# Kernel optimization log

Hardware: AMD Instinct MI355X
Metric: run time of the kernel (lower is better)

## Reference

```python
import jax, jax.numpy as jnp
import numpy as np

EPS = 1e-5       # InstanceNorm1d default eps
TEMP = 1.0       # temperature
SCALE = 8
# (name, arity) of the symbolic base, repeated SCALE times -> 48 functions, layer_size = 64
BASE = [("add", 2), ("mul", 2), ("sin", 1), ("cos", 1), ("tanh", 1), ("identity", 1)]


def _apply(name, a):
    if name == "add":
        return a[0] + a[1]
    if name == "mul":
        return a[0] * a[1]
    if name == "sin":
        return jnp.sin(a[0])
    if name == "cos":
        return jnp.cos(a[0])
    if name == "tanh":
        return jnp.tanh(a[0])
    return a[0]  # identity


def _inorm(x):
    # InstanceNorm1d, affine=False, biased variance, per (sample, channel) over L
    m = jnp.mean(x, axis=-1, keepdims=True)
    v = jnp.var(x, axis=-1, keepdims=True)
    return (x - m) * jax.lax.rsqrt(v + EPS)


def setup_inputs() -> dict:
    key = jax.random.key(0)
    k1, k2, k3 = jax.random.split(key, 3)
    x = jax.random.normal(k1, (64, 256, 4096), dtype=jnp.float32)
    w_channel = 0.1 * jax.random.normal(k2, (64, 256), dtype=jnp.float32)   # channel_conv 1x1
    w_down = 0.1 * jax.random.normal(k3, (48, 256), dtype=jnp.float32)      # down_conv 1x1
    return {"x": x, "w_channel": w_channel, "w_down": w_down}


def reference(x, w_channel, w_down):
    funcs = BASE * SCALE
    nx = _inorm(x)                                   # [B, C, L]
    # forward softmaxes channel_conv weight over output-channel dim (dim=0)
    w_eff = jax.nn.softmax(w_channel / TEMP, axis=0)  # [layer_size, C]
    multi = jnp.einsum("oc,bcl->bol", w_eff, nx)      # [B, layer_size, L]
    args_idx = 0
    output = None
    for i, (name, arity) in enumerate(funcs):
        args = [multi[:, args_idx + j : args_idx + j + 1] for j in range(arity)]
        img = _apply(name, args)                      # [B, 1, L]
        output = img if i == 0 else jnp.concatenate([output, img], axis=1)
        # original re-applies InstanceNorm to the growing tensor each iteration
        output = _inorm(output)
        args_idx += arity
    # skip connection
    output = output + jnp.einsum("oc,bcl->bol", w_down, nx)  # [B, 48, L]
    return output
```

## Files before the change

kernel.cpp:

```cpp
#include <hip/hip_runtime.h>
#include <hip/hip_bf16.h>

#define EPS 1e-5f

typedef unsigned int u32;
typedef unsigned short u16;
typedef __attribute__((ext_vector_type(8))) short bf16x8;
typedef __attribute__((ext_vector_type(4))) float f32x4;

__device__ __forceinline__ u32 f2bf(float f) {
    u32 u = __float_as_uint(f);
    u += 0x7FFFu + ((u >> 16) & 1u);
    return u >> 16;
}
__device__ __forceinline__ float bf2f(u32 h) {
    return __uint_as_float(h << 16);
}

__global__ __launch_bounds__(256) void k1_tstats(const float* __restrict__ x,
                                                 u16* __restrict__ xT,
                                                 float* __restrict__ gS,
                                                 float* __restrict__ gSS) {
    int b  = blockIdx.y;
    int c0 = (blockIdx.x & 7) * 32;
    int l0 = (blockIdx.x >> 3) * 512;
    int t  = threadIdx.x;
    __shared__ __align__(16) u16 T[512 * 32];

    int crow = t >> 3;
    int f4b  = t & 7;
    const float* xr = x + ((size_t)(b * 256 + c0 + crow)) * 4096 + l0;
    int cb   = (2 * crow) & 15;
    int slot = crow >> 3;
    float s = 0.f, ss = 0.f;
#pragma unroll
    for (int i = 0; i < 16; ++i) {
        int f4 = f4b + 8 * i;
        float4 v = *(const float4*)(xr + 4 * f4);
        s  += v.x + v.y + v.z + v.w;
        ss += v.x * v.x + v.y * v.y + v.z * v.z + v.w * v.w;
        char* base = (char*)T + f4 * 256 + (((slot ^ (f4 & 3)) << 4) | cb);
        *(u16*)(base      ) = (u16)f2bf(v.x);
        *(u16*)(base +  64) = (u16)f2bf(v.y);
        *(u16*)(base + 128) = (u16)f2bf(v.z);
        *(u16*)(base + 192) = (u16)f2bf(v.w);
    }
    s += __shfl_xor(s, 1, 64); ss += __shfl_xor(ss, 1, 64);
    s += __shfl_xor(s, 2, 64); ss += __shfl_xor(ss, 2, 64);
    s += __shfl_xor(s, 4, 64); ss += __shfl_xor(ss, 4, 64);
    if ((t & 7) == 0) {
        atomicAdd(&gS [b * 256 + c0 + crow], s);
        atomicAdd(&gSS[b * 256 + c0 + crow], ss);
    }
    __syncthreads();
    u16* xrow = xT + ((size_t)b * 4096 + l0) * 256 + c0;
    int sslot = t & 3;
#pragma unroll
    for (int k = 0; k < 8; ++k) {
        int ll  = k * 64 + (t >> 2);
        int key = (ll >> 2) & 3;
        uint4 vv = *(const uint4*)((const char*)T + ll * 64 + ((sslot ^ key) << 4));
        *(uint4*)(xrow + (size_t)ll * 256 + 8 * sslot) = vv;
    }
}

__global__ __launch_bounds__(256) void k2_prep(const float* __restrict__ wch,
                                               const float* __restrict__ wdn,
                                               const float* __restrict__ gS,
                                               const float* __restrict__ gSS,
                                               u16* __restrict__ Wc,
                                               float* __restrict__ bias,
                                               float* __restrict__ gsum,
                                               float* __restrict__ gss) {
    int b = blockIdx.x, t = threadIdx.x;
    __shared__ float smx[256], sinv[256], ssc[256], smn[256];
    {
        int c = t;
        float mx = -1e30f;
        for (int o = 0; o < 64; ++o) mx = fmaxf(mx, wch[o * 256 + c]);
        float sum = 0.f;
        for (int o = 0; o < 64; ++o) sum += __expf(wch[o * 256 + c] - mx);
        smx[c] = mx; sinv[c] = 1.f / sum;
        float S = gS[b * 256 + c], Q = gSS[b * 256 + c];
        float m = S * (1.f / 4096.f);
        float v = fmaxf(Q * (1.f / 4096.f) - m * m, 0.f);
        ssc[c] = rsqrtf(v + EPS);
        smn[c] = m;
    }
    __syncthreads();

    int lane = t & 63, w = t >> 6;
    int sub = lane >> 5, li = lane & 31;
    int c8 = li * 8;
    u16* Wb = Wc + (size_t)b * 128 * 256;
#pragma unroll 4
    for (int j = 0; j < 16; ++j) {
        int r = j * 8 + w * 2 + sub;
        float p = 0.f;
        u32 packed[4];
#pragma unroll
        for (int e = 0; e < 4; ++e) {
            u32 lohi[2];
#pragma unroll
            for (int h = 0; h < 2; ++h) {
                int c = c8 + 2 * e + h;
                float wv;
                if (r < 64)       wv = __expf(wch[r * 256 + c] - smx[c]) * sinv[c];
                else if (r < 112) wv = wdn[(r - 64) * 256 + c];
                else              wv = 0.f;
                u32 hb = f2bf(wv * ssc[c]);
                lohi[h] = hb;
                p += bf2f(hb) * smn[c];
            }
            packed[e] = lohi[0] | (lohi[1] << 16);
        }
        *(uint4*)&Wb[r * 256 + c8] = *(uint4*)packed;
#pragma unroll
        for (int off = 1; off <= 16; off <<= 1) p += __shfl_xor(p, off, 64);
        if (li == 0) bias[b * 128 + r] = -p;
    }
    if (t < 48) { gsum[b * 48 + t] = 0.f; gss[b * 48 + t] = 0.f; }
}

__global__ __launch_bounds__(256, 4) void k3_main(const u16* __restrict__ xT,
                                                  const u16* __restrict__ Wc,
                                                  const float* __restrict__ bias,
                                                  u16* __restrict__ imgw,
                                                  u16* __restrict__ skipw,
                                                  float* __restrict__ gsum,
                                                  float* __restrict__ gss) {
    int lt = blockIdx.x;
    int b  = blockIdx.y;
    int n0blk = lt * 128;
    int t = threadIdx.x;
    int w = t >> 6, u = t & 63;
    int lane16 = u & 15, q = u >> 4;
    int m0  = (w & 1) * 64;
    int n0w = (w >> 1) * 64;

    __shared__ __align__(16) u16 Wl[128 * 64];
    __shared__ __align__(16) u16 Xl[128 * 64];
    __shared__ float sbias[128];

    if (t < 128) sbias[t] = bias[b * 128 + t];

    f32x4 acc[4][4];
#pragma unroll
    for (int mt = 0; mt < 4; ++mt)
#pragma unroll
        for (int nt = 0; nt < 4; ++nt) acc[mt][nt] = (f32x4){0.f, 0.f, 0.f, 0.f};

    const char* Wb = (const char*)(Wc + (size_t)b * 128 * 256);
    const char* xb = (const char*)(xT + ((size_t)b * 4096 + n0blk) * 256);

    int r0   = t >> 3;
    int jb   = (t & 7) << 4;
    int swz0 = jb ^ (((t >> 3) & 7) << 4);
    int swz16 = (lane16 & 7) << 4;

    for (int cc = 0; cc < 4; ++cc) {
        if (cc) __syncthreads();
        int c0b = cc << 7;
#pragma unroll
        for (int p = 0; p < 4; ++p) {
            int r = r0 + 32 * p;
            uint4 wv = *(const uint4*)(Wb + (size_t)r * 512 + c0b + jb);
            uint4 xv = *(const uint4*)(xb + (size_t)r * 512 + c0b + jb);
            *(uint4*)((char*)Wl + r * 128 + swz0) = wv;
            *(uint4*)((char*)Xl + r * 128 + swz0) = xv;
        }
        __syncthreads();
#pragma unroll
        for (int kk = 0; kk < 2; ++kk) {
            int kob = (kk * 64 + q * 16) ^ swz16;
            bf16x8 af[4], bfr[4];
#pragma unroll
            for (int mt = 0; mt < 4; ++mt)
                af[mt] = *(const bf16x8*)((const char*)Wl + (m0 + 16 * mt + lane16) * 128 + kob);
#pragma unroll
            for (int nt = 0; nt < 4; ++nt)
                bfr[nt] = *(const bf16x8*)((const char*)Xl + (n0w + 16 * nt + lane16) * 128 + kob);
#pragma unroll
            for (int mt = 0; mt < 4; ++mt)
#pragma unroll
                for (int nt = 0; nt < 4; ++nt)
                    acc[mt][nt] = __builtin_amdgcn_mfma_f32_16x16x32_bf16(af[mt], bfr[nt], acc[mt][nt], 0, 0, 0);
        }
    }
    __syncthreads();

    int jb48 = b * 48;
    if (m0 == 0) {
        int g2 = q >> 1, qo = q & 1;
#pragma unroll
        for (int mt = 0; mt < 4; ++mt) {
            int g = 2 * mt + g2;
            int j0 = 6 * g + (qo ? 2 : 0);
            int cnt = qo ? 4 : 2;
            float b0 = sbias[16 * mt + 4 * q + 0];
            float b1 = sbias[16 * mt + 4 * q + 1];
            float b2 = sbias[16 * mt + 4 * q + 2];
            float b3 = sbias[16 * mt + 4 * q + 3];
            float sj[4] = {0.f, 0.f, 0.f, 0.f};
            float qj[4] = {0.f, 0.f, 0.f, 0.f};
#pragma unroll
            for (int nt = 0; nt < 4; ++nt) {
                f32x4 a = acc[mt][nt];
                float a0 = a[0] + b0, a1 = a[1] + b1, a2 = a[2] + b2, a3 = a[3] + b3;
                int n = n0blk + n0w + 16 * nt + lane16;
                float v[4];
                if (!qo) {
                    v[0] = a0 + a1;
                    v[1] = a2 * a3;
                    v[2] = 0.f; v[3] = 0.f;
                } else {
                    v[0] = __sinf(a0);
                    v[1] = __cosf(a1);
                    float e = __expf(-2.f * fabsf(a2));
                    v[2] = copysignf((1.f - e) / (1.f + e), a2);
                    v[3] = a3;
                }
                for (int i = 0; i < cnt; ++i) {
                    imgw[(size_t)(jb48 + j0 + i) * 4096 + n] = (u16)f2bf(v[i]);
                    sj[i] += v[i];
                    qj[i] += v[i] * v[i];
                }
            }
#pragma unroll
            for (int off = 1; off <= 8; off <<= 1) {
#pragma unroll
                for (int i = 0; i < 4; ++i) {
                    sj[i] += __shfl_xor(sj[i], off, 64);
                    qj[i] += __shfl_xor(qj[i], off, 64);
                }
            }
            if (lane16 == 0) {
                for (int i = 0; i < cnt; ++i) {
                    atomicAdd(&gsum[jb48 + j0 + i], sj[i]);
                    atomicAdd(&gss[jb48 + j0 + i],  qj[i]);
                }
            }
        }
    } else {
#pragma unroll
        for (int mt = 0; mt < 3; ++mt) {
            int j0 = 16 * mt + 4 * q;
            float b0 = sbias[64 + j0 + 0];
            float b1 = sbias[64 + j0 + 1];
            float b2 = sbias[64 + j0 + 2];
            float b3 = sbias[64 + j0 + 3];
#pragma unroll
            for (int nt = 0; nt < 4; ++nt) {
                f32x4 a = acc[mt][nt];
                int n = n0blk + n0w + 16 * nt + lane16;
                skipw[(size_t)(jb48 + j0 + 0) * 4096 + n] = (u16)f2bf(a[0] + b0);
                skipw[(size_t)(jb48 + j0 + 1) * 4096 + n] = (u16)f2bf(a[1] + b1);
                skipw[(size_t)(jb48 + j0 + 2) * 4096 + n] = (u16)f2bf(a[2] + b2);
                skipw[(size_t)(jb48 + j0 + 3) * 4096 + n] = (u16)f2bf(a[3] + b3);
            }
        }
    }
}

__global__ __launch_bounds__(256) void k4_final(const u16* __restrict__ imgw,
                                                const u16* __restrict__ skipw,
                                                const float* __restrict__ gsum,
                                                const float* __restrict__ gss,
                                                float* __restrict__ out) {
    int j = blockIdx.x, b = blockIdx.y;
    int bj = b * 48 + j;
    float m = gsum[bj] * (1.f / 4096.f);
    float v = fmaxf(gss[bj] * (1.f / 4096.f) - m * m, 0.f);
    float rs = rsqrtf(v + EPS);
    float g = 1.f;
    float vv = v / (v + EPS);
    for (int k = 0; k < 47 - j; ++k) {
        g *= rsqrtf(vv + EPS);
        vv = vv / (vv + EPS);
    }
    float sc = rs * g;
    const u16* ir = imgw  + (size_t)bj * 4096;
    const u16* sr = skipw + (size_t)bj * 4096;
    float* orow = out + (size_t)bj * 4096;
    int t = threadIdx.x;
#pragma unroll
    for (int i = 0; i < 2; ++i) {
        int idx = t * 8 + i * 2048;
        uint4 iv = *(const uint4*)(ir + idx);
        uint4 sv = *(const uint4*)(sr + idx);
        const u32* ih = (const u32*)&iv;
        const u32* sh = (const u32*)&sv;
        float o[8];
#pragma unroll
        for (int e = 0; e < 4; ++e) {
            float i_lo = bf2f(ih[e] & 0xFFFFu), i_hi = bf2f(ih[e] >> 16);
            float s_lo = bf2f(sh[e] & 0xFFFFu), s_hi = bf2f(sh[e] >> 16);
            o[2 * e]     = (i_lo - m) * sc + s_lo;
            o[2 * e + 1] = (i_hi - m) * sc + s_hi;
        }
        *(float4*)(orow + idx)     = make_float4(o[0], o[1], o[2], o[3]);
        *(float4*)(orow + idx + 4) = make_float4(o[4], o[5], o[6], o[7]);
    }
}

extern "C" void kernel_launch(void* const* d_in, const int* in_sizes, int n_in,
                              void* d_out, int out_size, void* d_ws, size_t ws_size,
                              hipStream_t stream) {
    const float* x   = (const float*)d_in[0];
    const float* wch = (const float*)d_in[1];
    const float* wdn = (const float*)d_in[2];
    float* out = (float*)d_out;

    float* gS    = (float*)d_ws;
    float* gSS   = gS + 16384;
    float* bias  = gSS + 16384;
    float* gsum  = bias + 64 * 128;
    float* gss   = gsum + 3072;
    u16*   Wc    = (u16*)(gss + 3072);
    u16*   xTw   = Wc + (size_t)64 * 128 * 256;
    u16*   imgw  = xTw + (size_t)64 * 4096 * 256;
    u16*   skipw = imgw + (size_t)64 * 48 * 4096;

    hipMemsetAsync(gS, 0, 2 * 16384 * sizeof(float), stream);
    k1_tstats<<<dim3(64, 64), dim3(256), 0, stream>>>(x, xTw, gS, gSS);
    k2_prep<<<dim3(64), dim3(256), 0, stream>>>(wch, wdn, gS, gSS, Wc, bias, gsum, gss);
    k3_main<<<dim3(32, 64), dim3(256), 0, stream>>>(xTw, Wc, bias, imgw, skipw, gsum, gss);
    k4_final<<<dim3(48, 64), dim3(256), 0, stream>>>(imgw, skipw, gsum, gss, out);
}
```

Baseline: 517.1 us.

## Use direct global-to-LDS loads in GEMM, drop atomics and memset for stats

```diff
diff --git a/kernel.cpp b/kernel.cpp
--- a/kernel.cpp
+++ b/kernel.cpp
@@ -15,6 +15,11 @@
 }
 __device__ __forceinline__ float bf2f(u32 h) {
     return __uint_as_float(h << 16);
+}
+
+__device__ __forceinline__ void gload16(const void* g, void* l) {
+    __builtin_amdgcn_global_load_lds((const __attribute__((address_space(1))) void*)g,
+                                     (__attribute__((address_space(3))) void*)l, 16, 0, 0);
 }
 
 __global__ __launch_bounds__(256) void k1_tstats(const float* __restrict__ x,
@@ -23,7 +28,8 @@
                                                  float* __restrict__ gSS) {
     int b  = blockIdx.y;
     int c0 = (blockIdx.x & 7) * 32;
-    int l0 = (blockIdx.x >> 3) * 512;
+    int lgrp = blockIdx.x >> 3;
+    int l0 = lgrp * 512;
     int t  = threadIdx.x;
     __shared__ __align__(16) u16 T[512 * 32];
 
@@ -49,8 +55,9 @@
     s += __shfl_xor(s, 2, 64); ss += __shfl_xor(ss, 2, 64);
     s += __shfl_xor(s, 4, 64); ss += __shfl_xor(ss, 4, 64);
     if ((t & 7) == 0) {
-        atomicAdd(&gS [b * 256 + c0 + crow], s);
-        atomicAdd(&gSS[b * 256 + c0 + crow], ss);
+        int idx = ((b * 256 + c0 + crow) << 3) + lgrp;
+        gS [idx] = s;
+        gSS[idx] = ss;
     }
     __syncthreads();
     u16* xrow = xT + ((size_t)b * 4096 + l0) * 256 + c0;
@@ -73,15 +80,24 @@
                                                float* __restrict__ gsum,
                                                float* __restrict__ gss) {
     int b = blockIdx.x, t = threadIdx.x;
-    __shared__ float smx[256], sinv[256], ssc[256], smn[256];
+    __shared__ float swch[64 * 256];
+    __shared__ float sinv[256], ssc[256], smn[256], smxs[256];
+#pragma unroll
+    for (int i = 0; i < 64; ++i) swch[i * 256 + t] = wch[i * 256 + t];
+    __syncthreads();
     {
         int c = t;
         float mx = -1e30f;
-        for (int o = 0; o < 64; ++o) mx = fmaxf(mx, wch[o * 256 + c]);
+        for (int o = 0; o < 64; ++o) mx = fmaxf(mx, swch[o * 256 + c]);
         float sum = 0.f;
-        for (int o = 0; o < 64; ++o) sum += __expf(wch[o * 256 + c] - mx);
-        smx[c] = mx; sinv[c] = 1.f / sum;
-        float S = gS[b * 256 + c], Q = gSS[b * 256 + c];
+        for (int o = 0; o < 64; ++o) sum += __expf(swch[o * 256 + c] - mx);
+        smxs[c] = mx; sinv[c] = 1.f / sum;
+        float S = 0.f, Q = 0.f;
+#pragma unroll
+        for (int k = 0; k < 8; ++k) {
+            S += gS [((b * 256 + c) << 3) + k];
+            Q += gSS[((b * 256 + c) << 3) + k];
+        }
         float m = S * (1.f / 4096.f);
         float v = fmaxf(Q * (1.f / 4096.f) - m * m, 0.f);
         ssc[c] = rsqrtf(v + EPS);
@@ -105,7 +121,7 @@
             for (int h = 0; h < 2; ++h) {
                 int c = c8 + 2 * e + h;
                 float wv;
-                if (r < 64)       wv = __expf(wch[r * 256 + c] - smx[c]) * sinv[c];
+                if (r < 64)       wv = __expf(swch[r * 256 + c] - smxs[c]) * sinv[c];
                 else if (r < 112) wv = wdn[(r - 64) * 256 + c];
                 else              wv = 0.f;
                 u32 hb = f2bf(wv * ssc[c]);
@@ -153,21 +169,22 @@
     const char* Wb = (const char*)(Wc + (size_t)b * 128 * 256);
     const char* xb = (const char*)(xT + ((size_t)b * 4096 + n0blk) * 256);
 
-    int r0   = t >> 3;
-    int jb   = (t & 7) << 4;
-    int swz0 = jb ^ (((t >> 3) & 7) << 4);
-    int swz16 = (lane16 & 7) << 4;
+    int r_lane = u >> 3;
+    int gswz   = ((u & 7) ^ r_lane) << 4;
+    int swz16  = (lane16 & 7) << 4;
 
     for (int cc = 0; cc < 4; ++cc) {
         if (cc) __syncthreads();
         int c0b = cc << 7;
 #pragma unroll
-        for (int p = 0; p < 4; ++p) {
-            int r = r0 + 32 * p;
-            uint4 wv = *(const uint4*)(Wb + (size_t)r * 512 + c0b + jb);
-            uint4 xv = *(const uint4*)(xb + (size_t)r * 512 + c0b + jb);
-            *(uint4*)((char*)Wl + r * 128 + swz0) = wv;
-            *(uint4*)((char*)Xl + r * 128 + swz0) = xv;
+        for (int k = 0; k < 4; ++k) {
+            int R0 = 32 * w + 8 * k;
+            gload16(Wb + (size_t)(R0 + r_lane) * 512 + c0b + gswz, (char*)Wl + R0 * 128);
+        }
+#pragma unroll
+        for (int k = 0; k < 4; ++k) {
+            int R0 = 32 * w + 8 * k;
+            gload16(xb + (size_t)(R0 + r_lane) * 512 + c0b + gswz, (char*)Xl + R0 * 128);
         }
         __syncthreads();
 #pragma unroll
@@ -175,11 +192,11 @@
             int kob = (kk * 64 + q * 16) ^ swz16;
             bf16x8 af[4], bfr[4];
 #pragma unroll
+            for (int nt = 0; nt < 4; ++nt)
+                bfr[nt] = *(const bf16x8*)((const char*)Xl + (n0w + 16 * nt + lane16) * 128 + kob);
+#pragma unroll
             for (int mt = 0; mt < 4; ++mt)
                 af[mt] = *(const bf16x8*)((const char*)Wl + (m0 + 16 * mt + lane16) * 128 + kob);
-#pragma unroll
-            for (int nt = 0; nt < 4; ++nt)
-                bfr[nt] = *(const bf16x8*)((const char*)Xl + (n0w + 16 * nt + lane16) * 128 + kob);
 #pragma unroll
             for (int mt = 0; mt < 4; ++mt)
 #pragma unroll
@@ -312,8 +329,8 @@
     float* out = (float*)d_out;
 
     float* gS    = (float*)d_ws;
-    float* gSS   = gS + 16384;
-    float* bias  = gSS + 16384;
+    float* gSS   = gS + 131072;
+    float* bias  = gSS + 131072;
     float* gsum  = bias + 64 * 128;
     float* gss   = gsum + 3072;
     u16*   Wc    = (u16*)(gss + 3072);
@@ -321,7 +338,6 @@
     u16*   imgw  = xTw + (size_t)64 * 4096 * 256;
     u16*   skipw = imgw + (size_t)64 * 48 * 4096;
 
-    hipMemsetAsync(gS, 0, 2 * 16384 * sizeof(float), stream);
     k1_tstats<<<dim3(64, 64), dim3(256), 0, stream>>>(x, xTw, gS, gSS);
     k2_prep<<<dim3(64), dim3(256), 0, stream>>>(wch, wdn, gS, gSS, Wc, bias, gsum, gss);
     k3_main<<<dim3(32, 64), dim3(256), 0, stream>>>(xTw, Wc, bias, imgw, skipw, gsum, gss);
```

Result: faster. 500.0 us (-3.3%).
